# Kernel tuning notes

Measured on AMD Instinct MI355X. Metric: run time of the kernel, lower is better.

Reference implementation:

```python
import jax, jax.numpy as jnp
import numpy as np

EPS = 1e-08
N_READS = 4
CELL_WIDTH = 64


def setup_inputs() -> dict:
    key = jax.random.key(0)
    ks = jax.random.split(key, 6)
    B, N, W, R = 8, 2048, CELL_WIDTH, N_READS
    memory = jax.random.normal(ks[0], (B, N, W), dtype=jnp.float32)
    controls = jax.random.normal(ks[1], (B, R * W + R + R * 3), dtype=jnp.float32)
    ww = jax.random.uniform(ks[2], (B, N), dtype=jnp.float32)
    write_weights = ww / ww.sum(-1, keepdims=True)  # simplex, as a DNC write head yields
    prev_links = jax.random.uniform(ks[3], (B, N, N), dtype=jnp.float32)
    prev_precedence = jax.random.uniform(ks[4], (B, N), dtype=jnp.float32)
    rw = jax.random.uniform(ks[5], (B, R, N), dtype=jnp.float32)
    prev_read_weights = rw / rw.sum(-1, keepdims=True)
    return {
        "memory": memory,
        "controls": controls,
        "write_weights": write_weights,
        "prev_links": prev_links,
        "prev_precedence": prev_precedence,
        "prev_read_weights": prev_read_weights,
    }


def reference(memory, controls, write_weights, prev_links, prev_precedence, prev_read_weights):
    B, N, W = memory.shape
    R = N_READS
    # --- split controls per self.shapes: [[R, W], R, [R, 3]] ---
    keys = controls[:, : R * W].reshape(B, R, W)
    betas = 1.0 + jax.nn.softplus(controls[:, R * W : R * W + R])  # [B, R]
    gates = jax.nn.softmax(controls[:, R * W + R :].reshape(B, R, 3), axis=-1)
    # --- content addressing: cosine similarity + softmax ---
    key_norm = jnp.linalg.norm(keys, axis=-1)    # [B, R]
    mem_norm = jnp.linalg.norm(memory, axis=-1)  # [B, N]
    dots = jnp.einsum("bnw,brw->brn", memory, keys)
    scores = dots / (key_norm[:, :, None] * mem_norm[:, None, :] + EPS)
    content_weights = jax.nn.softmax(scores * betas[:, :, None], axis=-1)  # [B, R, N]
    # --- temporal link matrix update ---
    wt_i = write_weights[:, :, None]          # [B, N, 1]
    wt_j = write_weights[:, None, :]          # [B, 1, N]
    pt_j = prev_precedence[:, None, :]        # [B, 1, N]
    diag_mask = 1.0 - jnp.eye(N, dtype=memory.dtype)
    links = ((1.0 - wt_i - wt_j) * prev_links + wt_i * pt_j) * diag_mask  # [B, N, N]
    # --- forward / backward weightings from prev read weights ---
    forward_weights = jnp.einsum("bij,brj->bri", links, prev_read_weights)
    backward_weights = jnp.einsum("bij,bri->brj", links, prev_read_weights)
    # --- mix via read modes ---
    read_weights = (
        gates[..., 0:1] * forward_weights
        + gates[..., 1:2] * backward_weights
        + gates[..., 2:3] * content_weights
    )  # [B, R, N]
    # --- read vector ---
    read_vector = jnp.einsum("bnw,brn->brw", memory, read_weights)  # [B, R, W]
    return read_vector
```

## Files before the change

kernel.cpp:

```cpp
#include <hip/hip_runtime.h>
#include <math.h>

#define BB 8
#define NN 2048
#define WWID 64
#define RNUM 4
#define CTRL 272
#define EPSF 1e-8f
#define TI 32
#define TILES 64

__device__ __forceinline__ float wred_sum(float v){
#pragma unroll
  for (int m=1;m<64;m<<=1) v += __shfl_xor(v,m);
  return v;
}
__device__ __forceinline__ float wred_max(float v){
#pragma unroll
  for (int m=1;m<64;m<<=1) v = fmaxf(v, __shfl_xor(v,m));
  return v;
}
__device__ __forceinline__ float block_sum(float v, float* sc8){
  int tid=threadIdx.x, wid=tid>>6, lane=tid&63;
  v = wred_sum(v);
  __syncthreads();
  if (lane==0) sc8[wid]=v;
  __syncthreads();
  return sc8[0]+sc8[1]+sc8[2]+sc8[3];
}
__device__ __forceinline__ float block_max(float v, float* sc8){
  int tid=threadIdx.x, wid=tid>>6, lane=tid&63;
  v = wred_max(v);
  __syncthreads();
  if (lane==0) sc8[wid]=v;
  __syncthreads();
  return fmaxf(fmaxf(sc8[0],sc8[1]),fmaxf(sc8[2],sc8[3]));
}

__global__ __launch_bounds__(256) void k1_prep(
    const float* __restrict__ mem, const float* __restrict__ ctr,
    const float* __restrict__ ww, const float* __restrict__ prw,
    float* __restrict__ dots, float* __restrict__ mem_norm,
    float* __restrict__ a_arr){
  int wid = threadIdx.x >> 6, lane = threadIdx.x & 63;
  int g = blockIdx.x * 4 + wid;
  int b = g >> 11, n = g & (NN-1);
  float m = mem[((size_t)(b*NN + n))*WWID + lane];
  const float* cb = ctr + b*CTRL;
  float s0 = m*m;
  float d0 = m * cb[0*WWID + lane];
  float d1 = m * cb[1*WWID + lane];
  float d2 = m * cb[2*WWID + lane];
  float d3 = m * cb[3*WWID + lane];
#pragma unroll
  for (int k=1;k<64;k<<=1){
    s0 += __shfl_xor(s0,k);
    d0 += __shfl_xor(d0,k);
    d1 += __shfl_xor(d1,k);
    d2 += __shfl_xor(d2,k);
    d3 += __shfl_xor(d3,k);
  }
  if (lane==0){
    mem_norm[b*NN+n] = sqrtf(s0);
    dots[(b*RNUM+0)*NN+n] = d0;
    dots[(b*RNUM+1)*NN+n] = d1;
    dots[(b*RNUM+2)*NN+n] = d2;
    dots[(b*RNUM+3)*NN+n] = d3;
  }
  if (lane < RNUM){
    int r = lane;
    a_arr[(b*RNUM+r)*NN+n] = (1.f - ww[b*NN+n]) * prw[(b*RNUM+r)*NN+n];
  }
}

__global__ __launch_bounds__(256) void k2_head(
    const float* __restrict__ ctr, const float* __restrict__ dots,
    const float* __restrict__ mem_norm, const float* __restrict__ ww,
    const float* __restrict__ prec, const float* __restrict__ prw,
    float* __restrict__ content, float* __restrict__ scal){
  __shared__ float sco[NN];
  __shared__ float sc8[8];
  __shared__ float vars[8];
  int tid = threadIdx.x;
  int b = blockIdx.x >> 2, r = blockIdx.x & 3;
  const float* cb = ctr + b*CTRL;
  if (tid < 64){
    float k = cb[r*WWID + tid];
    float kk = wred_sum(k*k);
    if (tid == 0){
      vars[0] = sqrtf(kk);
      float x = cb[RNUM*WWID + r];
      vars[1] = 1.f + (x > 20.f ? x : log1pf(expf(x)));
      float c0 = cb[RNUM*WWID + RNUM + r*3 + 0];
      float c1 = cb[RNUM*WWID + RNUM + r*3 + 1];
      float c2 = cb[RNUM*WWID + RNUM + r*3 + 2];
      float mg = fmaxf(c0, fmaxf(c1, c2));
      float e0 = expf(c0-mg), e1 = expf(c1-mg), e2 = expf(c2-mg);
      float inv = 1.f/(e0+e1+e2);
      vars[2]=e0*inv; vars[3]=e1*inv; vars[4]=e2*inv;
    }
  }
  __syncthreads();
  float knorm = vars[0], beta = vars[1];
  float lmax = -1e30f, lS = 0.f, lT = 0.f;
  for (int n=tid; n<NN; n+=256){
    float sc = dots[(b*RNUM+r)*NN+n] / (knorm*mem_norm[b*NN+n] + EPSF) * beta;
    sco[n] = sc;
    lmax = fmaxf(lmax, sc);
    float pr = prw[(b*RNUM+r)*NN+n];
    lS = fmaf(prec[b*NN+n], pr, lS);
    lT = fmaf(ww[b*NN+n],  pr, lT);
  }
  float mx = block_max(lmax, sc8);
  float S  = block_sum(lS, sc8);
  float T  = block_sum(lT, sc8);
  float lsum = 0.f;
  for (int n=tid; n<NN; n+=256){
    float e = expf(sco[n]-mx);
    sco[n] = e;
    lsum += e;
  }
  float sum = block_sum(lsum, sc8);
  float inv = 1.f/sum;
  for (int n=tid; n<NN; n+=256)
    content[(b*RNUM+r)*NN+n] = sco[n]*inv;
  if (tid == 0){
    float* s = &scal[(b*RNUM+r)*8];
    s[0]=vars[2]; s[1]=vars[3]; s[2]=vars[4]; s[3]=S; s[4]=T;
  }
}

__global__ __launch_bounds__(256) void k3_links(
    const float* __restrict__ L, const float* __restrict__ ww,
    const float* __restrict__ prw, const float* __restrict__ a_arr,
    float* __restrict__ fwd_raw, float* __restrict__ part){
  __shared__ float lrow[TI][16];
  __shared__ float lcol[256*16];
  int tid = threadIdx.x, wid = tid>>6, lane = tid&63;
  int b = blockIdx.x / TILES, tile = blockIdx.x % TILES;
  int i0 = tile*TI;
  if (tid < TI){
    int i = i0 + tid;
    lrow[tid][0] = ww[b*NN + i];
#pragma unroll
    for (int r=0;r<RNUM;r++){
      lrow[tid][4+r] = a_arr[(b*RNUM+r)*NN + i];
      lrow[tid][8+r] = prw[(b*RNUM+r)*NN + i];
    }
  }
  __syncthreads();
  float accf[8][4];
#pragma unroll
  for (int rr=0;rr<8;rr++)
#pragma unroll
    for (int r=0;r<4;r++) accf[rr][r]=0.f;

  for (int c=0;c<8;c++){
    int j0 = c*256 + lane*4;
    float4 a4[4], p4[4];
#pragma unroll
    for (int r=0;r<4;r++){
      a4[r] = *reinterpret_cast<const float4*>(&a_arr[(b*RNUM+r)*NN + j0]);
      p4[r] = *reinterpret_cast<const float4*>(&prw[(b*RNUM+r)*NN + j0]);
    }
    float4 wwj = *reinterpret_cast<const float4*>(&ww[b*NN + j0]);
    float4 cacc[4];
#pragma unroll
    for (int r=0;r<4;r++){ cacc[r].x=0.f; cacc[r].y=0.f; cacc[r].z=0.f; cacc[r].w=0.f; }

#pragma unroll
    for (int rr=0; rr<8; rr++){
      int lr = wid*8 + rr;
      int i  = i0 + lr;
      float wwi = lrow[lr][0];
      float4 ai4 = *reinterpret_cast<const float4*>(&lrow[lr][4]);
      float4 pi4 = *reinterpret_cast<const float4*>(&lrow[lr][8]);
      float4 L4 = *reinterpret_cast<const float4*>(&L[((size_t)(b*NN + i))*NN + j0]);
#pragma unroll
      for (int r=0;r<4;r++){
        float ax = (r==0)?a4[0].x:((r==1)?a4[1].x:((r==2)?a4[2].x:a4[3].x));
        float4 ar = a4[r], pr = p4[r];
        float mx_ = fmaf(-wwi, pr.x, ar.x);
        float my_ = fmaf(-wwi, pr.y, ar.y);
        float mz_ = fmaf(-wwi, pr.z, ar.z);
        float mw_ = fmaf(-wwi, pr.w, ar.w);
        float s = accf[rr][r];
        s = fmaf(L4.x, mx_, s); s = fmaf(L4.y, my_, s);
        s = fmaf(L4.z, mz_, s); s = fmaf(L4.w, mw_, s);
        accf[rr][r] = s;
        float ai = (r==0)?ai4.x:((r==1)?ai4.y:((r==2)?ai4.z:ai4.w));
        float pi = (r==0)?pi4.x:((r==1)?pi4.y:((r==2)?pi4.z:pi4.w));
        float nx_ = fmaf(-wwj.x, pi, ai);
        float ny_ = fmaf(-wwj.y, pi, ai);
        float nz_ = fmaf(-wwj.z, pi, ai);
        float nw_ = fmaf(-wwj.w, pi, ai);
        cacc[r].x = fmaf(L4.x, nx_, cacc[r].x);
        cacc[r].y = fmaf(L4.y, ny_, cacc[r].y);
        cacc[r].z = fmaf(L4.z, nz_, cacc[r].z);
        cacc[r].w = fmaf(L4.w, nw_, cacc[r].w);
        (void)ax;
      }
    }
    __syncthreads();
#pragma unroll
    for (int r=0;r<4;r++)
      *reinterpret_cast<float4*>(&lcol[tid*16 + r*4]) = cacc[r];
    __syncthreads();
    float4 v; v.x=0.f; v.y=0.f; v.z=0.f; v.w=0.f;
#pragma unroll
    for (int w=0;w<4;w++){
      float4 t = *reinterpret_cast<const float4*>(&lcol[(w*64+lane)*16 + wid*4]);
      v.x+=t.x; v.y+=t.y; v.z+=t.z; v.w+=t.w;
    }
    *reinterpret_cast<float4*>(
      &part[((size_t)((b*TILES+tile)*RNUM + wid))*NN + c*256 + lane*4]) = v;
  }
#pragma unroll
  for (int rr=0;rr<8;rr++){
#pragma unroll
    for (int r=0;r<4;r++){
      float v = wred_sum(accf[rr][r]);
      if (lane==0) fwd_raw[(b*RNUM+r)*NN + i0 + wid*8 + rr] = v;
    }
  }
}

__global__ __launch_bounds__(256) void k4_combine(
    const float* __restrict__ part, const float* __restrict__ fwd_raw,
    const float* __restrict__ content, const float* __restrict__ scal,
    const float* __restrict__ ww, const float* __restrict__ prec,
    const float* __restrict__ prw, const float* __restrict__ L,
    float* __restrict__ rw){
  int b = blockIdx.x >> 5, rem = blockIdx.x & 31;
  int r = rem >> 3, nb = rem & 7;
  int n = nb*256 + threadIdx.x;
  const float* s = &scal[(b*RNUM+r)*8];
  float g0=s[0], g1=s[1], g2=s[2], S=s[3], T=s[4];
  float bsum = 0.f;
  for (int t=0;t<TILES;t++)
    bsum += part[((size_t)((b*TILES+t)*RNUM + r))*NN + n];
  float wwn = ww[b*NN+n], pn = prec[b*NN+n], prn = prw[(b*RNUM+r)*NN+n];
  float Lnn = L[((size_t)(b*NN+n))*NN + n];
  float diag = (fmaf(-2.f*wwn, Lnn, Lnn) + wwn*pn) * prn;
  float fwd = fwd_raw[(b*RNUM+r)*NN+n] + wwn*S - diag;
  float bwd = bsum + pn*T - diag;
  rw[(b*RNUM+r)*NN+n] = g0*fwd + g1*bwd + g2*content[(b*RNUM+r)*NN+n];
}

__global__ __launch_bounds__(256) void k5_read(
    const float* __restrict__ mem, const float* __restrict__ rw,
    float* __restrict__ out){
  __shared__ float rwl[4][128];
  int tid = threadIdx.x;
  int b = blockIdx.x >> 4, ch = blockIdx.x & 15;
  int n0 = ch*128;
  for (int idx=tid; idx<512; idx+=256){
    int r = idx >> 7, nn = idx & 127;
    rwl[r][nn] = rw[(b*RNUM+r)*NN + n0 + nn];
  }
  __syncthreads();
  int wid = tid>>6, lane = tid&63;
  float acc = 0.f;
  for (int nn=0; nn<128; nn++)
    acc = fmaf(mem[((size_t)(b*NN + n0 + nn))*WWID + lane], rwl[wid][nn], acc);
  atomicAdd(&out[(b*RNUM+wid)*WWID + lane], acc);
}

extern "C" void kernel_launch(void* const* d_in, const int* in_sizes, int n_in,
                              void* d_out, int out_size, void* d_ws, size_t ws_size,
                              hipStream_t stream){
  const float* mem  = (const float*)d_in[0];
  const float* ctr  = (const float*)d_in[1];
  const float* ww   = (const float*)d_in[2];
  const float* L    = (const float*)d_in[3];
  const float* prec = (const float*)d_in[4];
  const float* prw  = (const float*)d_in[5];
  float* out = (float*)d_out;
  float* w = (float*)d_ws;

  float* dots     = w;
  float* mem_norm = dots + BB*RNUM*NN;
  float* a_arr    = mem_norm + BB*NN;
  float* content  = a_arr + BB*RNUM*NN;
  float* fwd_raw  = content + BB*RNUM*NN;
  float* scal     = fwd_raw + BB*RNUM*NN;
  float* rw       = scal + 256;
  float* part     = rw + BB*RNUM*NN;

  hipMemsetAsync(out, 0, (size_t)BB*RNUM*WWID*sizeof(float), stream);
  k1_prep<<<BB*NN/4, 256, 0, stream>>>(mem, ctr, ww, prw, dots, mem_norm, a_arr);
  k2_head<<<BB*RNUM, 256, 0, stream>>>(ctr, dots, mem_norm, ww, prec, prw, content, scal);
  k3_links<<<BB*TILES, 256, 0, stream>>>(L, ww, prw, a_arr, fwd_raw, part);
  k4_combine<<<BB*RNUM*8, 256, 0, stream>>>(part, fwd_raw, content, scal, ww, prec, prw, L, rw);
  k5_read<<<BB*16, 256, 0, stream>>>(mem, rw, out);
}
```

Measured before the change: 248.5 us.

## Split link kernel across column quarters, fold scores into prep, defer softmax normalization

The link-matrix kernel now splits each row tile into four column quarters, giving four times as many blocks, and writes partial forward sums that the combine kernel adds together. Cosine scores with beta scaling, and the diagonal of L, move into the prep kernel. The head kernel becomes a single 1024-thread reduction that only stores the max and inverse sum, with the softmax exponent deferred to the combine kernel. The reduction of forward sums is restructured as a transpose-style shuffle, the LDS layout is changed to avoid bank conflicts, and the read kernel uses smaller chunks with more blocks. The cost is more partial-sum traffic and more atomics in the final read.

```diff
diff --git a/kernel.cpp b/kernel.cpp
--- a/kernel.cpp
+++ b/kernel.cpp
@@ -9,6 +9,7 @@
 #define EPSF 1e-8f
 #define TI 32
 #define TILES 64
+#define CQ 4
 
 __device__ __forceinline__ float wred_sum(float v){
 #pragma unroll
@@ -19,53 +20,45 @@
 #pragma unroll
   for (int m=1;m<64;m<<=1) v = fmaxf(v, __shfl_xor(v,m));
   return v;
-}
-__device__ __forceinline__ float block_sum(float v, float* sc8){
-  int tid=threadIdx.x, wid=tid>>6, lane=tid&63;
-  v = wred_sum(v);
-  __syncthreads();
-  if (lane==0) sc8[wid]=v;
-  __syncthreads();
-  return sc8[0]+sc8[1]+sc8[2]+sc8[3];
-}
-__device__ __forceinline__ float block_max(float v, float* sc8){
-  int tid=threadIdx.x, wid=tid>>6, lane=tid&63;
-  v = wred_max(v);
-  __syncthreads();
-  if (lane==0) sc8[wid]=v;
-  __syncthreads();
-  return fmaxf(fmaxf(sc8[0],sc8[1]),fmaxf(sc8[2],sc8[3]));
 }
 
 __global__ __launch_bounds__(256) void k1_prep(
     const float* __restrict__ mem, const float* __restrict__ ctr,
     const float* __restrict__ ww, const float* __restrict__ prw,
-    float* __restrict__ dots, float* __restrict__ mem_norm,
-    float* __restrict__ a_arr){
+    const float* __restrict__ L,
+    float* __restrict__ scores, float* __restrict__ a_arr,
+    float* __restrict__ Ldiag){
   int wid = threadIdx.x >> 6, lane = threadIdx.x & 63;
   int g = blockIdx.x * 4 + wid;
   int b = g >> 11, n = g & (NN-1);
   float m = mem[((size_t)(b*NN + n))*WWID + lane];
   const float* cb = ctr + b*CTRL;
+  float k0 = cb[0*WWID+lane], k1 = cb[1*WWID+lane];
+  float k2 = cb[2*WWID+lane], k3 = cb[3*WWID+lane];
   float s0 = m*m;
-  float d0 = m * cb[0*WWID + lane];
-  float d1 = m * cb[1*WWID + lane];
-  float d2 = m * cb[2*WWID + lane];
-  float d3 = m * cb[3*WWID + lane];
-#pragma unroll
-  for (int k=1;k<64;k<<=1){
-    s0 += __shfl_xor(s0,k);
-    d0 += __shfl_xor(d0,k);
-    d1 += __shfl_xor(d1,k);
-    d2 += __shfl_xor(d2,k);
-    d3 += __shfl_xor(d3,k);
+  float d0 = m*k0, d1 = m*k1, d2 = m*k2, d3 = m*k3;
+  float q0 = k0*k0, q1 = k1*k1, q2 = k2*k2, q3 = k3*k3;
+#pragma unroll
+  for (int t=1;t<64;t<<=1){
+    s0 += __shfl_xor(s0,t);
+    d0 += __shfl_xor(d0,t); d1 += __shfl_xor(d1,t);
+    d2 += __shfl_xor(d2,t); d3 += __shfl_xor(d3,t);
+    q0 += __shfl_xor(q0,t); q1 += __shfl_xor(q1,t);
+    q2 += __shfl_xor(q2,t); q3 += __shfl_xor(q3,t);
   }
   if (lane==0){
-    mem_norm[b*NN+n] = sqrtf(s0);
-    dots[(b*RNUM+0)*NN+n] = d0;
-    dots[(b*RNUM+1)*NN+n] = d1;
-    dots[(b*RNUM+2)*NN+n] = d2;
-    dots[(b*RNUM+3)*NN+n] = d3;
+    float mn = sqrtf(s0);
+    float be[4];
+#pragma unroll
+    for (int r=0;r<4;r++){
+      float x = cb[RNUM*WWID + r];
+      be[r] = 1.f + (x > 20.f ? x : log1pf(expf(x)));
+    }
+    scores[(b*RNUM+0)*NN+n] = d0*be[0]/(sqrtf(q0)*mn + EPSF);
+    scores[(b*RNUM+1)*NN+n] = d1*be[1]/(sqrtf(q1)*mn + EPSF);
+    scores[(b*RNUM+2)*NN+n] = d2*be[2]/(sqrtf(q2)*mn + EPSF);
+    scores[(b*RNUM+3)*NN+n] = d3*be[3]/(sqrtf(q3)*mn + EPSF);
+    Ldiag[b*NN+n] = L[((size_t)(b*NN+n))*NN + n];
   }
   if (lane < RNUM){
     int r = lane;
@@ -73,72 +66,59 @@
   }
 }
 
-__global__ __launch_bounds__(256) void k2_head(
-    const float* __restrict__ ctr, const float* __restrict__ dots,
-    const float* __restrict__ mem_norm, const float* __restrict__ ww,
-    const float* __restrict__ prec, const float* __restrict__ prw,
-    float* __restrict__ content, float* __restrict__ scal){
-  __shared__ float sco[NN];
-  __shared__ float sc8[8];
-  __shared__ float vars[8];
-  int tid = threadIdx.x;
+__global__ __launch_bounds__(1024) void k2_head(
+    const float* __restrict__ ctr, const float* __restrict__ scores,
+    const float* __restrict__ ww, const float* __restrict__ prec,
+    const float* __restrict__ prw, float* __restrict__ scal){
+  __shared__ float redm[16], redS[16], redT[16], reds[16];
+  int tid = threadIdx.x, wid = tid>>6, lane = tid&63;
   int b = blockIdx.x >> 2, r = blockIdx.x & 3;
-  const float* cb = ctr + b*CTRL;
-  if (tid < 64){
-    float k = cb[r*WWID + tid];
-    float kk = wred_sum(k*k);
-    if (tid == 0){
-      vars[0] = sqrtf(kk);
-      float x = cb[RNUM*WWID + r];
-      vars[1] = 1.f + (x > 20.f ? x : log1pf(expf(x)));
-      float c0 = cb[RNUM*WWID + RNUM + r*3 + 0];
-      float c1 = cb[RNUM*WWID + RNUM + r*3 + 1];
-      float c2 = cb[RNUM*WWID + RNUM + r*3 + 2];
-      float mg = fmaxf(c0, fmaxf(c1, c2));
-      float e0 = expf(c0-mg), e1 = expf(c1-mg), e2 = expf(c2-mg);
-      float inv = 1.f/(e0+e1+e2);
-      vars[2]=e0*inv; vars[3]=e1*inv; vars[4]=e2*inv;
-    }
-  }
-  __syncthreads();
-  float knorm = vars[0], beta = vars[1];
-  float lmax = -1e30f, lS = 0.f, lT = 0.f;
-  for (int n=tid; n<NN; n+=256){
-    float sc = dots[(b*RNUM+r)*NN+n] / (knorm*mem_norm[b*NN+n] + EPSF) * beta;
-    sco[n] = sc;
-    lmax = fmaxf(lmax, sc);
-    float pr = prw[(b*RNUM+r)*NN+n];
-    lS = fmaf(prec[b*NN+n], pr, lS);
-    lT = fmaf(ww[b*NN+n],  pr, lT);
-  }
-  float mx = block_max(lmax, sc8);
-  float S  = block_sum(lS, sc8);
-  float T  = block_sum(lT, sc8);
-  float lsum = 0.f;
-  for (int n=tid; n<NN; n+=256){
-    float e = expf(sco[n]-mx);
-    sco[n] = e;
-    lsum += e;
-  }
-  float sum = block_sum(lsum, sc8);
-  float inv = 1.f/sum;
-  for (int n=tid; n<NN; n+=256)
-    content[(b*RNUM+r)*NN+n] = sco[n]*inv;
-  if (tid == 0){
+  const float* sc = scores + (size_t)(b*RNUM+r)*NN;
+  const float* pr = prw    + (size_t)(b*RNUM+r)*NN;
+  float s0 = sc[tid], s1 = sc[tid+1024];
+  float p0 = pr[tid], p1 = pr[tid+1024];
+  float lmax = fmaxf(s0, s1);
+  float lS = prec[b*NN+tid]*p0 + prec[b*NN+tid+1024]*p1;
+  float lT = ww[b*NN+tid]*p0   + ww[b*NN+tid+1024]*p1;
+  lmax = wred_max(lmax); lS = wred_sum(lS); lT = wred_sum(lT);
+  if (lane==0){ redm[wid]=lmax; redS[wid]=lS; redT[wid]=lT; }
+  __syncthreads();
+  float mx=-1e30f, S=0.f, T=0.f;
+#pragma unroll
+  for (int i=0;i<16;i++){ mx=fmaxf(mx,redm[i]); S+=redS[i]; T+=redT[i]; }
+  float ls = expf(s0-mx) + expf(s1-mx);
+  ls = wred_sum(ls);
+  if (lane==0) reds[wid]=ls;
+  __syncthreads();
+  float sum=0.f;
+#pragma unroll
+  for (int i=0;i<16;i++) sum += reds[i];
+  if (tid==0){
+    const float* cb = ctr + b*CTRL;
+    float c0 = cb[RNUM*WWID + RNUM + r*3 + 0];
+    float c1 = cb[RNUM*WWID + RNUM + r*3 + 1];
+    float c2 = cb[RNUM*WWID + RNUM + r*3 + 2];
+    float mg = fmaxf(c0, fmaxf(c1, c2));
+    float e0 = expf(c0-mg), e1 = expf(c1-mg), e2 = expf(c2-mg);
+    float inv3 = 1.f/(e0+e1+e2);
     float* s = &scal[(b*RNUM+r)*8];
-    s[0]=vars[2]; s[1]=vars[3]; s[2]=vars[4]; s[3]=S; s[4]=T;
+    s[0]=e0*inv3; s[1]=e1*inv3; s[2]=e2*inv3;
+    s[3]=S; s[4]=T; s[5]=mx; s[6]=1.f/sum;
   }
 }
 
 __global__ __launch_bounds__(256) void k3_links(
     const float* __restrict__ L, const float* __restrict__ ww,
     const float* __restrict__ prw, const float* __restrict__ a_arr,
-    float* __restrict__ fwd_raw, float* __restrict__ part){
+    float* __restrict__ fwd_part, float* __restrict__ part){
   __shared__ float lrow[TI][16];
-  __shared__ float lcol[256*16];
+  __shared__ float lcol[4096];
   int tid = threadIdx.x, wid = tid>>6, lane = tid&63;
-  int b = blockIdx.x / TILES, tile = blockIdx.x % TILES;
-  int i0 = tile*TI;
+  int bid = blockIdx.x;
+  int b   = bid >> 8;
+  int rem = bid & 255;
+  int tile = rem >> 2, cq = rem & 3;
+  int i0 = tile*TI, jbase = cq*512;
   if (tid < TI){
     int i = i0 + tid;
     lrow[tid][0] = ww[b*NN + i];
@@ -149,14 +129,12 @@
     }
   }
   __syncthreads();
-  float accf[8][4];
-#pragma unroll
-  for (int rr=0;rr<8;rr++)
-#pragma unroll
-    for (int r=0;r<4;r++) accf[rr][r]=0.f;
-
-  for (int c=0;c<8;c++){
-    int j0 = c*256 + lane*4;
+  float accf[32];
+#pragma unroll
+  for (int k=0;k<32;k++) accf[k]=0.f;
+
+  for (int c=0;c<2;c++){
+    int j0 = jbase + c*256 + lane*4;
     float4 a4[4], p4[4];
 #pragma unroll
     for (int r=0;r<4;r++){
@@ -178,16 +156,15 @@
       float4 L4 = *reinterpret_cast<const float4*>(&L[((size_t)(b*NN + i))*NN + j0]);
 #pragma unroll
       for (int r=0;r<4;r++){
-        float ax = (r==0)?a4[0].x:((r==1)?a4[1].x:((r==2)?a4[2].x:a4[3].x));
         float4 ar = a4[r], pr = p4[r];
         float mx_ = fmaf(-wwi, pr.x, ar.x);
         float my_ = fmaf(-wwi, pr.y, ar.y);
         float mz_ = fmaf(-wwi, pr.z, ar.z);
         float mw_ = fmaf(-wwi, pr.w, ar.w);
-        float s = accf[rr][r];
+        float s = accf[rr*4+r];
         s = fmaf(L4.x, mx_, s); s = fmaf(L4.y, my_, s);
         s = fmaf(L4.z, mz_, s); s = fmaf(L4.w, mw_, s);
-        accf[rr][r] = s;
+        accf[rr*4+r] = s;
         float ai = (r==0)?ai4.x:((r==1)?ai4.y:((r==2)?ai4.z:ai4.w));
         float pi = (r==0)?pi4.x:((r==1)?pi4.y:((r==2)?pi4.z:pi4.w));
         float nx_ = fmaf(-wwj.x, pi, ai);
@@ -198,71 +175,90 @@
         cacc[r].y = fmaf(L4.y, ny_, cacc[r].y);
         cacc[r].z = fmaf(L4.z, nz_, cacc[r].z);
         cacc[r].w = fmaf(L4.w, nw_, cacc[r].w);
-        (void)ax;
       }
     }
     __syncthreads();
 #pragma unroll
     for (int r=0;r<4;r++)
-      *reinterpret_cast<float4*>(&lcol[tid*16 + r*4]) = cacc[r];
+      *reinterpret_cast<float4*>(&lcol[wid*1024 + r*256 + lane*4]) = cacc[r];
     __syncthreads();
     float4 v; v.x=0.f; v.y=0.f; v.z=0.f; v.w=0.f;
 #pragma unroll
     for (int w=0;w<4;w++){
-      float4 t = *reinterpret_cast<const float4*>(&lcol[(w*64+lane)*16 + wid*4]);
+      float4 t = *reinterpret_cast<const float4*>(&lcol[w*1024 + wid*256 + lane*4]);
       v.x+=t.x; v.y+=t.y; v.z+=t.z; v.w+=t.w;
     }
     *reinterpret_cast<float4*>(
-      &part[((size_t)((b*TILES+tile)*RNUM + wid))*NN + c*256 + lane*4]) = v;
-  }
-#pragma unroll
-  for (int rr=0;rr<8;rr++){
-#pragma unroll
-    for (int r=0;r<4;r++){
-      float v = wred_sum(accf[rr][r]);
-      if (lane==0) fwd_raw[(b*RNUM+r)*NN + i0 + wid*8 + rr] = v;
-    }
+      &part[((size_t)((b*TILES+tile)*RNUM + wid))*NN + jbase + c*256 + lane*4]) = v;
+  }
+
+#pragma unroll
+  for (int k=0;k<32;k++) accf[k] += __shfl_xor(accf[k], 32);
+#pragma unroll
+  for (int h=16; h>=1; h>>=1){
+#pragma unroll
+    for (int i=0;i<h;i++){
+      float a = accf[i], bb = accf[i+h];
+      bool up = (lane & h) != 0;
+      float lo = up ? bb : a;
+      float hi = up ? a : bb;
+      accf[i] = lo + __shfl_xor(hi, h);
+    }
+  }
+  if (lane < 32){
+    int k = lane;
+    fwd_part[((size_t)(b*CQ + cq)*RNUM + (k&3))*NN + i0 + wid*8 + (k>>2)] = accf[0];
   }
 }
 
 __global__ __launch_bounds__(256) void k4_combine(
-    const float* __restrict__ part, const float* __restrict__ fwd_raw,
-    const float* __restrict__ content, const float* __restrict__ scal,
+    const float* __restrict__ part, const float* __restrict__ fwd_part,
+    const float* __restrict__ scores, const float* __restrict__ scal,
     const float* __restrict__ ww, const float* __restrict__ prec,
-    const float* __restrict__ prw, const float* __restrict__ L,
+    const float* __restrict__ prw, const float* __restrict__ Ldiag,
     float* __restrict__ rw){
   int b = blockIdx.x >> 5, rem = blockIdx.x & 31;
   int r = rem >> 3, nb = rem & 7;
   int n = nb*256 + threadIdx.x;
   const float* s = &scal[(b*RNUM+r)*8];
-  float g0=s[0], g1=s[1], g2=s[2], S=s[3], T=s[4];
-  float bsum = 0.f;
-  for (int t=0;t<TILES;t++)
-    bsum += part[((size_t)((b*TILES+t)*RNUM + r))*NN + n];
+  float g0=s[0], g1=s[1], g2=s[2], S=s[3], T=s[4], mx=s[5], inv=s[6];
+  const float* pp = part + ((size_t)(b*TILES)*RNUM + r)*NN + n;
+  float b0=0.f,b1=0.f,b2=0.f,b3=0.f;
+  for (int t=0;t<TILES;t+=4){
+    b0 += pp[(size_t)(t+0)*RNUM*NN];
+    b1 += pp[(size_t)(t+1)*RNUM*NN];
+    b2 += pp[(size_t)(t+2)*RNUM*NN];
+    b3 += pp[(size_t)(t+3)*RNUM*NN];
+  }
+  float bsum = (b0+b1)+(b2+b3);
+  float fsum = 0.f;
+#pragma unroll
+  for (int cq=0;cq<CQ;cq++)
+    fsum += fwd_part[((size_t)(b*CQ + cq)*RNUM + r)*NN + n];
   float wwn = ww[b*NN+n], pn = prec[b*NN+n], prn = prw[(b*RNUM+r)*NN+n];
-  float Lnn = L[((size_t)(b*NN+n))*NN + n];
+  float Lnn = Ldiag[b*NN+n];
   float diag = (fmaf(-2.f*wwn, Lnn, Lnn) + wwn*pn) * prn;
-  float fwd = fwd_raw[(b*RNUM+r)*NN+n] + wwn*S - diag;
+  float fwd = fsum + wwn*S - diag;
   float bwd = bsum + pn*T - diag;
-  rw[(b*RNUM+r)*NN+n] = g0*fwd + g1*bwd + g2*content[(b*RNUM+r)*NN+n];
+  float content = expf(scores[(b*RNUM+r)*NN+n] - mx) * inv;
+  rw[(b*RNUM+r)*NN+n] = g0*fwd + g1*bwd + g2*content;
 }
 
 __global__ __launch_bounds__(256) void k5_read(
     const float* __restrict__ mem, const float* __restrict__ rw,
     float* __restrict__ out){
-  __shared__ float rwl[4][128];
+  __shared__ float rwl[256];
   int tid = threadIdx.x;
-  int b = blockIdx.x >> 4, ch = blockIdx.x & 15;
-  int n0 = ch*128;
-  for (int idx=tid; idx<512; idx+=256){
-    int r = idx >> 7, nn = idx & 127;
-    rwl[r][nn] = rw[(b*RNUM+r)*NN + n0 + nn];
-  }
+  int b = blockIdx.x >> 5, ch = blockIdx.x & 31;
+  int n0 = ch*64;
+  int r = tid >> 6, nn = tid & 63;
+  rwl[tid] = rw[(b*RNUM+r)*NN + n0 + nn];
   __syncthreads();
   int wid = tid>>6, lane = tid&63;
   float acc = 0.f;
-  for (int nn=0; nn<128; nn++)
-    acc = fmaf(mem[((size_t)(b*NN + n0 + nn))*WWID + lane], rwl[wid][nn], acc);
+#pragma unroll 4
+  for (int q=0; q<64; q++)
+    acc = fmaf(mem[((size_t)(b*NN + n0 + q))*WWID + lane], rwl[wid*64+q], acc);
   atomicAdd(&out[(b*RNUM+wid)*WWID + lane], acc);
 }
 
@@ -278,19 +274,18 @@
   float* out = (float*)d_out;
   float* w = (float*)d_ws;
 
-  float* dots     = w;
-  float* mem_norm = dots + BB*RNUM*NN;
-  float* a_arr    = mem_norm + BB*NN;
-  float* content  = a_arr + BB*RNUM*NN;
-  float* fwd_raw  = content + BB*RNUM*NN;
-  float* scal     = fwd_raw + BB*RNUM*NN;
-  float* rw       = scal + 256;
+  float* scores   = w;
+  float* a_arr    = scores + BB*RNUM*NN;
+  float* Ldiag    = a_arr + BB*RNUM*NN;
+  float* scal     = Ldiag + BB*NN;
+  float* fwd_part = scal + 256;
+  float* rw       = fwd_part + BB*CQ*RNUM*NN;
   float* part     = rw + BB*RNUM*NN;
 
   hipMemsetAsync(out, 0, (size_t)BB*RNUM*WWID*sizeof(float), stream);
-  k1_prep<<<BB*NN/4, 256, 0, stream>>>(mem, ctr, ww, prw, dots, mem_norm, a_arr);
-  k2_head<<<BB*RNUM, 256, 0, stream>>>(ctr, dots, mem_norm, ww, prec, prw, content, scal);
-  k3_links<<<BB*TILES, 256, 0, stream>>>(L, ww, prw, a_arr, fwd_raw, part);
-  k4_combine<<<BB*RNUM*8, 256, 0, stream>>>(part, fwd_raw, content, scal, ww, prec, prw, L, rw);
-  k5_read<<<BB*16, 256, 0, stream>>>(mem, rw, out);
-}
+  k1_prep<<<BB*NN/4, 256, 0, stream>>>(mem, ctr, ww, prw, L, scores, a_arr, Ldiag);
+  k2_head<<<BB*RNUM, 1024, 0, stream>>>(ctr, scores, ww, prec, prw, scal);
+  k3_links<<<BB*TILES*CQ, 256, 0, stream>>>(L, ww, prw, a_arr, fwd_part, part);
+  k4_combine<<<BB*RNUM*8, 256, 0, stream>>>(part, fwd_part, scores, scal, ww, prec, prw, Ldiag, rw);
+  k5_read<<<BB*32, 256, 0, stream>>>(mem, rw, out);
+}
```

Measured after the change: 252.7 us. About the same (+1.7%).
